# Optimization experiments

Measured on AMD Instinct MI355X. Metric: run time of the kernel, lower is better.

Reference implementation:

```python
import jax, jax.numpy as jnp
import numpy as np

N, C, H, W = 32, 256, 64, 64
K = 1024  # embed_size


def setup_inputs() -> dict:
    key = jax.random.key(0)
    k1, k2 = jax.random.split(key)
    x = jax.random.normal(k1, (N, C, H, W), dtype=jnp.float32)
    embed = jax.random.normal(k2, (K, C), dtype=jnp.float32)  # codebook buffer
    return {"x": x, "embed": embed}


def reference(x, embed):
    n, c, h, w = x.shape
    # [N,C,H,W] -> [N*H*W, C]
    flat = jnp.transpose(x, (0, 2, 3, 1)).reshape(-1, c)
    # squared euclidean distance; sqrt omitted since argmin is invariant
    d = (
        jnp.sum(flat * flat, axis=-1, keepdims=True)
        - 2.0 * flat @ embed.T
        + jnp.sum(embed * embed, axis=-1)
    )  # [N*H*W, K]
    embed_idx = jnp.argmin(d, axis=1).reshape(n, h, w)
    quantize = embed[embed_idx]  # [N,H,W,C]
    quantize = jnp.transpose(quantize, (0, 3, 1, 2))  # [N,C,H,W]
    diff = jnp.mean((jax.lax.stop_gradient(quantize) - x) ** 2)
    quantize = x + jax.lax.stop_gradient(quantize - x)  # straight-through
    return quantize, embed_idx, diff
```

## Files before the change

### kernel.cpp

```cpp
#include <hip/hip_runtime.h>

#define NB    32
#define CDIM  256
#define HWSZ  4096
#define NPOS  (NB*HWSZ)
#define KCODES 1024
#define QELEMS ((size_t)NB*CDIM*HWSZ)
#define IDX_OFF QELEMS
#define DIFF_OFF (QELEMS + NPOS)
#define EBYTES (32*32768)
#define E2F_OFF (EBYTES/4)

#define X2P   65536
#define X2T   67584
#define MVOFF 67840
#define MIOFF 69888
#define LDSSZ 71936

typedef _Float16       f16x8  __attribute__((ext_vector_type(8)));
typedef float          f32x16 __attribute__((ext_vector_type(16)));
typedef unsigned short u16x8  __attribute__((ext_vector_type(8)));

static __device__ inline unsigned short f2h(float f) {
    _Float16 h = (_Float16)f;
    return __builtin_bit_cast(unsigned short, h);
}

__global__ __launch_bounds__(64) void vq_prep_embed(const float* __restrict__ embed,
                                                    float* __restrict__ out) {
    const int k = blockIdx.x;
    const int lane = threadIdx.x;
    const float4 v = *reinterpret_cast<const float4*>(embed + (size_t)k * CDIM + lane * 4);

    unsigned char* __restrict__ ebuf = (unsigned char*)out;

    _Float16 h0 = (_Float16)v.x, h1 = (_Float16)v.y, h2 = (_Float16)v.z, h3 = (_Float16)v.w;
    ushort4 hv = { __builtin_bit_cast(unsigned short, h0), __builtin_bit_cast(unsigned short, h1),
                   __builtin_bit_cast(unsigned short, h2), __builtin_bit_cast(unsigned short, h3) };
    ushort4 lv = { f2h((v.x - (float)h0) * 64.0f), f2h((v.y - (float)h1) * 64.0f),
                   f2h((v.z - (float)h2) * 64.0f), f2h((v.w - (float)h3) * 64.0f) };

    const int c0  = lane * 4;
    const int r   = c0 >> 4;
    const int hi  = (c0 >> 3) & 1;
    const int sub = c0 & 7;
    const size_t byte = (size_t)r * 32768 + (size_t)k * 32 + hi * 16 + sub * 2;
    *reinterpret_cast<ushort4*>(ebuf + byte)              = hv;
    *reinterpret_cast<ushort4*>(ebuf + byte + 16 * 32768) = lv;

    float s = v.x * v.x + v.y * v.y + v.z * v.z + v.w * v.w;
    #pragma unroll
    for (int m = 1; m < 64; m <<= 1) s += __shfl_xor(s, m, 64);
    if (lane == 0) out[E2F_OFF + k] = s;
    if (k == 0 && lane == 0) out[DIFF_OFF] = 0.0f;
}

__global__ __launch_bounds__(512) void vq_stage1(const float* __restrict__ x,
                                                 float* __restrict__ out) {
    __shared__ __align__(16) unsigned char lds[LDSSZ];

    const unsigned char* __restrict__ ebuf = (const unsigned char*)out;
    const float* __restrict__ e2buf = out + E2F_OFF;
    float* __restrict__ idx_out = out + IDX_OFF;

    const int t     = threadIdx.x;
    const int lane  = t & 63;
    const int col32 = lane & 31;
    const int hi    = lane >> 5;
    const int widx  = t >> 6;

    const int pos0 = blockIdx.x * 64;
    const int n    = pos0 >> 12;
    const int hw0  = pos0 & 4095;
    const float* __restrict__ xbase = x + (size_t)n * (CDIM * HWSZ) + hw0;

    {
        const int i = t & 63;
        const int g = t >> 6;
        float x2p = 0.f;
        #pragma unroll
        for (int j = 0; j < 4; ++j) {
            const int c0 = g * 32 + j * 8;
            u16x8 hv, lv;
            #pragma unroll
            for (int q = 0; q < 8; ++q) {
                float vv = xbase[(size_t)(c0 + q) * HWSZ + i];
                x2p = fmaf(vv, vv, x2p);
                _Float16 hh = (_Float16)vv;
                hv[q] = __builtin_bit_cast(unsigned short, hh);
                lv[q] = f2h((vv - (float)hh) * 64.0f);
            }
            const int kc = c0 >> 4;
            const int kh = (c0 >> 3) & 1;
            const int byte = kc * 2048 + kh * 1024 + i * 16;
            *reinterpret_cast<u16x8*>(lds + byte)         = hv;
            *reinterpret_cast<u16x8*>(lds + byte + 32768) = lv;
        }
        ((float*)(lds + X2P))[g * 64 + i] = x2p;
    }
    __syncthreads();

    if (t < 64) {
        const float* p = (const float*)(lds + X2P);
        float s = 0.f;
        #pragma unroll
        for (int g = 0; g < 8; ++g) s += p[g * 64 + t];
        ((float*)(lds + X2T))[t] = s;
    }
    __syncthreads();

    f32x16 acc[2][4];
    #pragma unroll
    for (int ra = 0; ra < 2; ++ra)
        #pragma unroll
        for (int cb = 0; cb < 4; ++cb)
            #pragma unroll
            for (int r = 0; r < 16; ++r) acc[ra][cb][r] = 0.f;

    const int aoff = hi * 1024 + col32 * 16;
    const unsigned char* __restrict__ bbase =
        ebuf + (size_t)widx * 4096 + (size_t)col32 * 32 + (size_t)hi * 16;

    #pragma unroll 2
    for (int kq = 0; kq < 48; ++kq) {
        const int seg = kq >> 4;
        const int r   = (kq < 32) ? kq : (kq - 32);
        const unsigned char* ab = lds + (kq & 15) * 2048 + ((seg == 2) ? 32768 : 0);
        const unsigned char* bp = bbase + (size_t)r * 32768;

        f16x8 a0 = *reinterpret_cast<const f16x8*>(ab + aoff);
        f16x8 a1 = *reinterpret_cast<const f16x8*>(ab + aoff + 512);
        f16x8 b0 = *reinterpret_cast<const f16x8*>(bp);
        f16x8 b1 = *reinterpret_cast<const f16x8*>(bp + 1024);
        f16x8 b2 = *reinterpret_cast<const f16x8*>(bp + 2048);
        f16x8 b3 = *reinterpret_cast<const f16x8*>(bp + 3072);

        if (seg == 1) {
            a0 *= (_Float16)0.015625f;
            a1 *= (_Float16)0.015625f;
        } else if (seg == 2) {
            b0 *= (_Float16)0.015625f;
            b1 *= (_Float16)0.015625f;
            b2 *= (_Float16)0.015625f;
            b3 *= (_Float16)0.015625f;
        }

        __builtin_amdgcn_s_setprio(1);
        acc[0][0] = __builtin_amdgcn_mfma_f32_32x32x16_f16(a0, b0, acc[0][0], 0, 0, 0);
        acc[0][1] = __builtin_amdgcn_mfma_f32_32x32x16_f16(a0, b1, acc[0][1], 0, 0, 0);
        acc[0][2] = __builtin_amdgcn_mfma_f32_32x32x16_f16(a0, b2, acc[0][2], 0, 0, 0);
        acc[0][3] = __builtin_amdgcn_mfma_f32_32x32x16_f16(a0, b3, acc[0][3], 0, 0, 0);
        acc[1][0] = __builtin_amdgcn_mfma_f32_32x32x16_f16(a1, b0, acc[1][0], 0, 0, 0);
        acc[1][1] = __builtin_amdgcn_mfma_f32_32x32x16_f16(a1, b1, acc[1][1], 0, 0, 0);
        acc[1][2] = __builtin_amdgcn_mfma_f32_32x32x16_f16(a1, b2, acc[1][2], 0, 0, 0);
        acc[1][3] = __builtin_amdgcn_mfma_f32_32x32x16_f16(a1, b3, acc[1][3], 0, 0, 0);
        __builtin_amdgcn_s_setprio(0);
    }

    const float* x2t = (const float*)(lds + X2T);
    float e2v[4];
    #pragma unroll
    for (int cb = 0; cb < 4; ++cb)
        e2v[cb] = e2buf[widx * 128 + cb * 32 + col32];

    float* mv = (float*)(lds + MVOFF);
    int*   mi = (int*)(lds + MIOFF);

    #pragma unroll
    for (int ra = 0; ra < 2; ++ra) {
        #pragma unroll
        for (int reg = 0; reg < 16; ++reg) {
            const int pos = ra * 32 + (reg & 3) + 8 * (reg >> 2) + 4 * hi;
            const float x2 = x2t[pos];
            float bv_ = 3.4e38f;
            int   bi_ = 0;
            #pragma unroll
            for (int cb = 0; cb < 4; ++cb) {
                const int code = widx * 128 + cb * 32 + col32;
                const float s = (x2 - 2.0f * acc[ra][cb][reg]) + e2v[cb];
                if (s < bv_) { bv_ = s; bi_ = code; }
            }
            #pragma unroll
            for (int m = 1; m < 32; m <<= 1) {
                float ov = __shfl_xor(bv_, m, 64);
                int   oi = __shfl_xor(bi_, m, 64);
                if (ov < bv_ || (ov == bv_ && oi < bi_)) { bv_ = ov; bi_ = oi; }
            }
            if (col32 == 0) {
                mv[widx * 64 + pos] = bv_;
                mi[widx * 64 + pos] = bi_;
            }
        }
    }

    __syncthreads();
    if (t < 64) {
        float bv_ = mv[t];
        int   bi_ = mi[t];
        #pragma unroll
        for (int w = 1; w < 8; ++w) {
            const float ov = mv[w * 64 + t];
            const int   oi = mi[w * 64 + t];
            if (ov < bv_ || (ov == bv_ && oi < bi_)) { bv_ = ov; bi_ = oi; }
        }
        idx_out[pos0 + t] = (float)bi_;
        float d = bv_;
        #pragma unroll
        for (int m = 1; m < 64; m <<= 1) d += __shfl_xor(d, m, 64);
        if (t == 0) atomicAdd(out + DIFF_OFF, d * (1.0f / 33554432.0f));
    }
}

__global__ __launch_bounds__(256) void vq_gather_kernel(const float* __restrict__ embed,
                                                        float* __restrict__ out) {
    const int tid = threadIdx.x;
    const int p = blockIdx.x * 256 + tid;
    const int n = p >> 12;
    const int hw = p & 4095;
    const int idx = (int)out[IDX_OFF + p];
    const float4* __restrict__ erow4 = reinterpret_cast<const float4*>(embed + (size_t)idx * CDIM);
    float* __restrict__ op = out + (size_t)n * (CDIM * HWSZ) + hw;

    #pragma unroll 8
    for (int c4 = 0; c4 < 64; ++c4) {
        const float4 e = erow4[c4];
        op[(size_t)(c4 * 4 + 0) * HWSZ] = e.x;
        op[(size_t)(c4 * 4 + 1) * HWSZ] = e.y;
        op[(size_t)(c4 * 4 + 2) * HWSZ] = e.z;
        op[(size_t)(c4 * 4 + 3) * HWSZ] = e.w;
    }
}

extern "C" void kernel_launch(void* const* d_in, const int* in_sizes, int n_in,
                              void* d_out, int out_size, void* d_ws, size_t ws_size,
                              hipStream_t stream) {
    const float* x = (const float*)d_in[0];
    const float* embed = (const float*)d_in[1];
    float* out = (float*)d_out;

    vq_prep_embed<<<KCODES, 64, 0, stream>>>(embed, out);
    vq_stage1<<<NPOS / 64, 512, 0, stream>>>(x, out);
    vq_gather_kernel<<<NPOS / 256, 256, 0, stream>>>(embed, out);
}
```

Baseline: 413.3 us.

## Split codebook across 16 waves with precomputed scaled fp16 operands and B prefetch

```diff
diff --git a/kernel.cpp b/kernel.cpp
--- a/kernel.cpp
+++ b/kernel.cpp
@@ -8,14 +8,14 @@
 #define QELEMS ((size_t)NB*CDIM*HWSZ)
 #define IDX_OFF QELEMS
 #define DIFF_OFF (QELEMS + NPOS)
-#define EBYTES (32*32768)
+#define EBYTES (48*32768)
 #define E2F_OFF (EBYTES/4)
 
-#define X2P   65536
-#define X2T   67584
-#define MVOFF 67840
-#define MIOFF 69888
-#define LDSSZ 71936
+#define X2P   98304
+#define X2T   102400
+#define MVOFF 102656
+#define MIOFF 106752
+#define LDSSZ 110848
 
 typedef _Float16       f16x8  __attribute__((ext_vector_type(8)));
 typedef float          f32x16 __attribute__((ext_vector_type(16)));
@@ -39,14 +39,17 @@
                    __builtin_bit_cast(unsigned short, h2), __builtin_bit_cast(unsigned short, h3) };
     ushort4 lv = { f2h((v.x - (float)h0) * 64.0f), f2h((v.y - (float)h1) * 64.0f),
                    f2h((v.z - (float)h2) * 64.0f), f2h((v.w - (float)h3) * 64.0f) };
+    ushort4 hv64 = { f2h((float)h0 * 0.015625f), f2h((float)h1 * 0.015625f),
+                     f2h((float)h2 * 0.015625f), f2h((float)h3 * 0.015625f) };
 
     const int c0  = lane * 4;
-    const int r   = c0 >> 4;
-    const int hi  = (c0 >> 3) & 1;
+    const int kc  = c0 >> 4;
+    const int kh  = (c0 >> 3) & 1;
     const int sub = c0 & 7;
-    const size_t byte = (size_t)r * 32768 + (size_t)k * 32 + hi * 16 + sub * 2;
+    const size_t byte = (size_t)kc * 32768 + (size_t)k * 32 + kh * 16 + sub * 2;
     *reinterpret_cast<ushort4*>(ebuf + byte)              = hv;
     *reinterpret_cast<ushort4*>(ebuf + byte + 16 * 32768) = lv;
+    *reinterpret_cast<ushort4*>(ebuf + byte + 32 * 32768) = hv64;
 
     float s = v.x * v.x + v.y * v.y + v.z * v.z + v.w * v.w;
     #pragma unroll
@@ -55,8 +58,8 @@
     if (k == 0 && lane == 0) out[DIFF_OFF] = 0.0f;
 }
 
-__global__ __launch_bounds__(512) void vq_stage1(const float* __restrict__ x,
-                                                 float* __restrict__ out) {
+__global__ __launch_bounds__(1024) void vq_stage1(const float* __restrict__ x,
+                                                  float* __restrict__ out) {
     __shared__ __align__(16) unsigned char lds[LDSSZ];
 
     const unsigned char* __restrict__ ebuf = (const unsigned char*)out;
@@ -79,22 +82,22 @@
         const int g = t >> 6;
         float x2p = 0.f;
         #pragma unroll
-        for (int j = 0; j < 4; ++j) {
-            const int c0 = g * 32 + j * 8;
-            u16x8 hv, lv;
+        for (int j = 0; j < 2; ++j) {
+            const int c0 = g * 16 + j * 8;
+            u16x8 hv, lv, hv64;
             #pragma unroll
             for (int q = 0; q < 8; ++q) {
                 float vv = xbase[(size_t)(c0 + q) * HWSZ + i];
                 x2p = fmaf(vv, vv, x2p);
                 _Float16 hh = (_Float16)vv;
-                hv[q] = __builtin_bit_cast(unsigned short, hh);
-                lv[q] = f2h((vv - (float)hh) * 64.0f);
+                hv[q]   = __builtin_bit_cast(unsigned short, hh);
+                lv[q]   = f2h((vv - (float)hh) * 64.0f);
+                hv64[q] = f2h((float)hh * 0.015625f);
             }
-            const int kc = c0 >> 4;
-            const int kh = (c0 >> 3) & 1;
-            const int byte = kc * 2048 + kh * 1024 + i * 16;
+            const int byte = g * 2048 + j * 1024 + i * 16;
             *reinterpret_cast<u16x8*>(lds + byte)         = hv;
-            *reinterpret_cast<u16x8*>(lds + byte + 32768) = lv;
+            *reinterpret_cast<u16x8*>(lds + byte + 32768) = hv64;
+            *reinterpret_cast<u16x8*>(lds + byte + 65536) = lv;
         }
         ((float*)(lds + X2P))[g * 64 + i] = x2p;
     }
@@ -104,64 +107,49 @@
         const float* p = (const float*)(lds + X2P);
         float s = 0.f;
         #pragma unroll
-        for (int g = 0; g < 8; ++g) s += p[g * 64 + t];
+        for (int g = 0; g < 16; ++g) s += p[g * 64 + t];
         ((float*)(lds + X2T))[t] = s;
     }
     __syncthreads();
 
-    f32x16 acc[2][4];
-    #pragma unroll
-    for (int ra = 0; ra < 2; ++ra)
-        #pragma unroll
-        for (int cb = 0; cb < 4; ++cb)
-            #pragma unroll
-            for (int r = 0; r < 16; ++r) acc[ra][cb][r] = 0.f;
+    f32x16 acc00 = {}, acc01 = {}, acc10 = {}, acc11 = {};
 
     const int aoff = hi * 1024 + col32 * 16;
-    const unsigned char* __restrict__ bbase =
-        ebuf + (size_t)widx * 4096 + (size_t)col32 * 32 + (size_t)hi * 16;
-
-    #pragma unroll 2
-    for (int kq = 0; kq < 48; ++kq) {
-        const int seg = kq >> 4;
-        const int r   = (kq < 32) ? kq : (kq - 32);
-        const unsigned char* ab = lds + (kq & 15) * 2048 + ((seg == 2) ? 32768 : 0);
-        const unsigned char* bp = bbase + (size_t)r * 32768;
-
-        f16x8 a0 = *reinterpret_cast<const f16x8*>(ab + aoff);
-        f16x8 a1 = *reinterpret_cast<const f16x8*>(ab + aoff + 512);
-        f16x8 b0 = *reinterpret_cast<const f16x8*>(bp);
-        f16x8 b1 = *reinterpret_cast<const f16x8*>(bp + 1024);
-        f16x8 b2 = *reinterpret_cast<const f16x8*>(bp + 2048);
-        f16x8 b3 = *reinterpret_cast<const f16x8*>(bp + 3072);
-
-        if (seg == 1) {
-            a0 *= (_Float16)0.015625f;
-            a1 *= (_Float16)0.015625f;
-        } else if (seg == 2) {
-            b0 *= (_Float16)0.015625f;
-            b1 *= (_Float16)0.015625f;
-            b2 *= (_Float16)0.015625f;
-            b3 *= (_Float16)0.015625f;
-        }
-
+    const unsigned char* __restrict__ bl =
+        ebuf + (size_t)((widx * 64 + col32) * 32 + hi * 16);
+
+    auto bload = [&](int kq, int cb) {
+        return *reinterpret_cast<const f16x8*>(bl + (size_t)kq * 32768 + cb * 1024);
+    };
+    auto aload = [&](int kq, int ra) {
+        return *reinterpret_cast<const f16x8*>(
+            lds + (kq >> 4) * 32768 + (kq & 15) * 2048 + aoff + ra * 512);
+    };
+
+    f16x8 b0 = bload(0, 0), b1 = bload(0, 1);
+    for (int kq = 0; kq < 48; kq += 2) {
+        f16x8 b0n = bload(kq + 1, 0), b1n = bload(kq + 1, 1);
+        f16x8 a0 = aload(kq, 0), a1 = aload(kq, 1);
         __builtin_amdgcn_s_setprio(1);
-        acc[0][0] = __builtin_amdgcn_mfma_f32_32x32x16_f16(a0, b0, acc[0][0], 0, 0, 0);
-        acc[0][1] = __builtin_amdgcn_mfma_f32_32x32x16_f16(a0, b1, acc[0][1], 0, 0, 0);
-        acc[0][2] = __builtin_amdgcn_mfma_f32_32x32x16_f16(a0, b2, acc[0][2], 0, 0, 0);
-        acc[0][3] = __builtin_amdgcn_mfma_f32_32x32x16_f16(a0, b3, acc[0][3], 0, 0, 0);
-        acc[1][0] = __builtin_amdgcn_mfma_f32_32x32x16_f16(a1, b0, acc[1][0], 0, 0, 0);
-        acc[1][1] = __builtin_amdgcn_mfma_f32_32x32x16_f16(a1, b1, acc[1][1], 0, 0, 0);
-        acc[1][2] = __builtin_amdgcn_mfma_f32_32x32x16_f16(a1, b2, acc[1][2], 0, 0, 0);
-        acc[1][3] = __builtin_amdgcn_mfma_f32_32x32x16_f16(a1, b3, acc[1][3], 0, 0, 0);
+        acc00 = __builtin_amdgcn_mfma_f32_32x32x16_f16(a0, b0, acc00, 0, 0, 0);
+        acc01 = __builtin_amdgcn_mfma_f32_32x32x16_f16(a0, b1, acc01, 0, 0, 0);
+        acc10 = __builtin_amdgcn_mfma_f32_32x32x16_f16(a1, b0, acc10, 0, 0, 0);
+        acc11 = __builtin_amdgcn_mfma_f32_32x32x16_f16(a1, b1, acc11, 0, 0, 0);
         __builtin_amdgcn_s_setprio(0);
+
+        b0 = bload(kq + 2, 0); b1 = bload(kq + 2, 1);
+        f16x8 a0n = aload(kq + 1, 0), a1n = aload(kq + 1, 1);
+        __builtin_amdgcn_s_setprio(1);
+        acc00 = __builtin_amdgcn_mfma_f32_32x32x16_f16(a0n, b0n, acc00, 0, 0, 0);
+        acc01 = __builtin_amdgcn_mfma_f32_32x32x16_f16(a0n, b1n, acc01, 0, 0, 0);
+        acc10 = __builtin_amdgcn_mfma_f32_32x32x16_f16(a1n, b0n, acc10, 0, 0, 0);
+        acc11 = __builtin_amdgcn_mfma_f32_32x32x16_f16(a1n, b1n, acc11, 0, 0, 0);
+        __builtin_amdgcn_s_setprio(0);
     }
 
     const float* x2t = (const float*)(lds + X2T);
-    float e2v[4];
-    #pragma unroll
-    for (int cb = 0; cb < 4; ++cb)
-        e2v[cb] = e2buf[widx * 128 + cb * 32 + col32];
+    const float e2v0 = e2buf[widx * 64 + col32];
+    const float e2v1 = e2buf[widx * 64 + 32 + col32];
 
     float* mv = (float*)(lds + MVOFF);
     int*   mi = (int*)(lds + MIOFF);
@@ -172,14 +160,13 @@
         for (int reg = 0; reg < 16; ++reg) {
             const int pos = ra * 32 + (reg & 3) + 8 * (reg >> 2) + 4 * hi;
             const float x2 = x2t[pos];
-            float bv_ = 3.4e38f;
-            int   bi_ = 0;
-            #pragma unroll
-            for (int cb = 0; cb < 4; ++cb) {
-                const int code = widx * 128 + cb * 32 + col32;
-                const float s = (x2 - 2.0f * acc[ra][cb][reg]) + e2v[cb];
-                if (s < bv_) { bv_ = s; bi_ = code; }
-            }
+            const float d0 = (ra == 0) ? acc00[reg] : acc10[reg];
+            const float d1 = (ra == 0) ? acc01[reg] : acc11[reg];
+            float bv_ = (x2 - 2.0f * d0) + e2v0;
+            int   bi_ = widx * 64 + col32;
+            const float s1 = (x2 - 2.0f * d1) + e2v1;
+            const int   c1 = widx * 64 + 32 + col32;
+            if (s1 < bv_) { bv_ = s1; bi_ = c1; }
             #pragma unroll
             for (int m = 1; m < 32; m <<= 1) {
                 float ov = __shfl_xor(bv_, m, 64);
@@ -198,7 +185,7 @@
         float bv_ = mv[t];
         int   bi_ = mi[t];
         #pragma unroll
-        for (int w = 1; w < 8; ++w) {
+        for (int w = 1; w < 16; ++w) {
             const float ov = mv[w * 64 + t];
             const int   oi = mi[w * 64 + t];
             if (ov < bv_ || (ov == bv_ && oi < bi_)) { bv_ = ov; bi_ = oi; }
@@ -239,6 +226,6 @@
     float* out = (float*)d_out;
 
     vq_prep_embed<<<KCODES, 64, 0, stream>>>(embed, out);
-    vq_stage1<<<NPOS / 64, 512, 0, stream>>>(x, out);
+    vq_stage1<<<NPOS / 64, 1024, 0, stream>>>(x, out);
     vq_gather_kernel<<<NPOS / 256, 256, 0, stream>>>(embed, out);
 }
```

Measured after the change: 388.3 us. 1.06x faster.
